# Optimization experiments

Measured on AMD Instinct MI355X. Metric: run time of the kernel, lower is better.

The kernel has to match this reference:

```python
import jax, jax.numpy as jnp
import numpy as np

N = 100000
E = 3200000
G = 64  # number of graphs


def _lin_params(key, fan_in, fan_out):
    k1, k2 = jax.random.split(key)
    bound = 1.0 / np.sqrt(fan_in)
    W = jax.random.uniform(k1, (fan_in, fan_out), jnp.float32, -bound, bound)
    b = jax.random.uniform(k2, (fan_out,), jnp.float32, -bound, bound)
    return W, b


def setup_inputs() -> dict:
    key = jax.random.key(0)
    ks = jax.random.split(key, 12)
    x = jax.random.normal(ks[0], (N, 3), jnp.float32)
    edge_index = jax.random.randint(ks[1], (2, E), 0, N, jnp.int32)
    batch = jnp.sort(jax.random.randint(ks[2], (N,), 0, G, jnp.int32))
    # conv1: in=3, heads=4, out_channels=16, concat=True -> 64
    Wq1, bq1 = _lin_params(ks[3], 3, 64)
    Wk1, bk1 = _lin_params(ks[4], 3, 64)
    Wv1, bv1 = _lin_params(ks[5], 3, 64)
    Ws1, bs1 = _lin_params(ks[6], 3, 64)
    # conv2: in=64, heads=1, out_channels=6, concat=False -> 6
    Wq2, bq2 = _lin_params(ks[7], 64, 6)
    Wk2, bk2 = _lin_params(ks[8], 64, 6)
    Wv2, bv2 = _lin_params(ks[9], 64, 6)
    Ws2, bs2 = _lin_params(ks[10], 64, 6)
    return dict(x=x, edge_index=edge_index, batch=batch,
                Wq1=Wq1, bq1=bq1, Wk1=Wk1, bk1=bk1, Wv1=Wv1, bv1=bv1, Ws1=Ws1, bs1=bs1,
                Wq2=Wq2, bq2=bq2, Wk2=Wk2, bk2=bk2, Wv2=Wv2, bv2=bv2, Ws2=Ws2, bs2=bs2)


def transformer_conv(x, src, dst, Wq, bq, Wk, bk, Wv, bv, Ws, bs, heads, d, concat):
    n = x.shape[0]
    q = (x @ Wq + bq).reshape(n, heads, d)
    k = (x @ Wk + bk).reshape(n, heads, d)
    v = (x @ Wv + bv).reshape(n, heads, d)
    # per-edge attention logits: query at target, key at source  [E, H]
    logits = jnp.einsum('ehd,ehd->eh', q[dst], k[src]) / jnp.sqrt(jnp.float32(d))
    # segment softmax over incoming edges of each target node
    m = jax.ops.segment_max(logits, dst, num_segments=n)          # [N, H]
    a = jnp.exp(logits - m[dst])                                   # [E, H]
    denom = jax.ops.segment_sum(a, dst, num_segments=n)           # [N, H]
    alpha = a / (denom[dst] + 1e-16)
    out = jax.ops.segment_sum(alpha[:, :, None] * v[src], dst, num_segments=n)  # [N,H,d]
    out = out.reshape(n, heads * d) if concat else out.mean(axis=1)
    return out + x @ Ws + bs  # root/skip connection


def reference(x, edge_index, batch,
              Wq1, bq1, Wk1, bk1, Wv1, bv1, Ws1, bs1,
              Wq2, bq2, Wk2, bk2, Wv2, bv2, Ws2, bs2):
    src, dst = edge_index[0], edge_index[1]
    h = transformer_conv(x, src, dst, Wq1, bq1, Wk1, bk1, Wv1, bv1, Ws1, bs1,
                         heads=4, d=16, concat=True)
    h = jax.nn.relu(h)
    # dropout is identity in eval mode
    h = transformer_conv(h, src, dst, Wq2, bq2, Wk2, bk2, Wv2, bv2, Ws2, bs2,
                         heads=1, d=6, concat=False)
    # global mean pool over graphs
    sums = jax.ops.segment_sum(h, batch, num_segments=G)
    cnts = jax.ops.segment_sum(jnp.ones((h.shape[0],), h.dtype), batch, num_segments=G)
    pooled = sums / jnp.maximum(cnts, 1.0)[:, None]
    return jax.nn.log_softmax(pooled, axis=1)
```

## Files before the change

### kernel.cpp

```cpp
#include <hip/hip_runtime.h>
#include <hip/hip_fp16.h>
#include <math.h>

#define N_NODES 100000
#define N_EDGES 3200000
#define N_GRAPHS 64
#define NEG_INF -1e30f

#define NB 196
#define CAP 18432
#define NBLK 1024
#define CHUNK 3125

__device__ __forceinline__ void atomAddF(float* p, float v) {
#if defined(__HIP_PLATFORM_AMD__)
    unsafeAtomicAdd(p, v);
#else
    atomicAdd(p, v);
#endif
}

__device__ __forceinline__ float b2f(unsigned w, int sh) {
    return (float)(signed char)(w >> sh);
}

__device__ __forceinline__ float kvdot(const float* q, uint4 w, float* sv_out) {
    float2 s = __half22float2(*(const __half2*)&w.w);
    *sv_out = s.y;
    return s.x * (q[0] * b2f(w.x, 0) + q[1] * b2f(w.x, 8)
                + q[2] * b2f(w.x, 16) + q[3] * b2f(w.x, 24)
                + q[4] * b2f(w.y, 0) + q[5] * b2f(w.y, 8));
}

__global__ void k0_packx(const float* __restrict__ x, float4* __restrict__ xp,
                         uint2* __restrict__ xh) {
    int n = blockIdx.x * 256 + threadIdx.x;
    if (n >= N_NODES) return;
    float x0 = x[3 * n], x1 = x[3 * n + 1], x2 = x[3 * n + 2];
    xp[n] = make_float4(x0, x1, x2, 0.f);
    __half2 h01 = __floats2half2_rn(x0, x1);
    __half2 h2p = __floats2half2_rn(x2, 0.f);
    xh[n] = make_uint2(*(unsigned*)&h01, *(unsigned*)&h2p);
}

__global__ void s1_partition(const int* __restrict__ ei,
                             int* __restrict__ bucket_fill,
                             unsigned* __restrict__ pairs) {
    __shared__ int cnt[NB];
    __shared__ int cur[NB];
    for (int i = threadIdx.x; i < NB; i += 256) cnt[i] = 0;
    __syncthreads();
    int base = blockIdx.x * CHUNK;
    for (int i = threadIdx.x; i < CHUNK; i += 256) {
        unsigned dst = (unsigned)ei[N_EDGES + base + i];
        atomicAdd(&cnt[dst >> 9], 1);
    }
    __syncthreads();
    for (int b = threadIdx.x; b < NB; b += 256) {
        int c = cnt[b];
        int off = c > 0 ? atomicAdd(&bucket_fill[b], c) : 0;
        cur[b] = b * CAP + off;
    }
    __syncthreads();
    for (int i = threadIdx.x; i < CHUNK; i += 256) {
        unsigned dst = (unsigned)ei[N_EDGES + base + i];
        int src = ei[base + i];
        int pos = atomicAdd(&cur[dst >> 9], 1);
        pairs[pos] = ((unsigned)src << 9) | (dst & 511u);
    }
}

__global__ void b4_build(const unsigned* __restrict__ pairs,
                         const int* __restrict__ bucket_fill,
                         int* __restrict__ rs, int* __restrict__ re,
                         int* __restrict__ csr_src) {
    __shared__ int cnt[512];
    __shared__ int sc[512];
    __shared__ int cur[512];
    int b = blockIdx.x;
    int tid = threadIdx.x;
    int rbase = b * CAP;
    int ne = bucket_fill[b];

    cnt[tid] = 0;
    __syncthreads();
    for (int i = tid; i < ne; i += 512)
        atomicAdd(&cnt[pairs[rbase + i] & 511u], 1);
    __syncthreads();
    sc[tid] = cnt[tid];
    __syncthreads();
    for (int off = 1; off < 512; off <<= 1) {
        int v = (tid >= off) ? sc[tid - off] : 0;
        __syncthreads();
        sc[tid] += v;
        __syncthreads();
    }
    int excl = sc[tid] - cnt[tid];
    cur[tid] = rbase + excl;
    int node = (b << 9) + tid;
    if (node < N_NODES) {
        rs[node] = rbase + excl;
        re[node] = rbase + sc[tid];
    }
    __syncthreads();
    for (int i = tid; i < ne; i += 512) {
        unsigned p = pairs[rbase + i];
        int pos = atomicAdd(&cur[p & 511u], 1);
        csr_src[pos] = (int)(p >> 9);
    }
}

__global__ void g1_layer1(const float4* __restrict__ xp,
                          const uint2* __restrict__ xh,
                          const float* __restrict__ Wq, const float* __restrict__ bq,
                          const float* __restrict__ Wk, const float* __restrict__ bk,
                          const float* __restrict__ Wv, const float* __restrict__ bv,
                          const float* __restrict__ Ws, const float* __restrict__ bs,
                          const int* __restrict__ rs, const int* __restrict__ re,
                          const int* __restrict__ csr_src,
                          uint2* __restrict__ h1) {
    __shared__ float sWq[192], sWk[192], sWv[192], sWs[192];
    __shared__ float sbq[64], sbk[64], sbv[64], sbs[64];
    for (int i = threadIdx.x; i < 192; i += 256) {
        sWq[i] = Wq[i]; sWk[i] = Wk[i]; sWv[i] = Wv[i]; sWs[i] = Ws[i];
    }
    for (int i = threadIdx.x; i < 64; i += 256) {
        sbq[i] = bq[i]; sbk[i] = bk[i]; sbv[i] = bv[i]; sbs[i] = bs[i];
    }
    __syncthreads();

    int lane = threadIdx.x & 63;
    int u = lane & 15;
    int slot = u >> 2;
    int j0 = u * 4;
    int n = blockIdx.x * 16 + (threadIdx.x >> 6) * 4 + (lane >> 4);

    float4 xc = xp[n];
    float x0 = xc.x, x1 = xc.y, x2 = xc.z;

    float q[4];
#pragma unroll
    for (int i = 0; i < 4; ++i)
        q[i] = 0.25f * (sbq[j0 + i] + x0 * sWq[j0 + i] + x1 * sWq[64 + j0 + i]
                        + x2 * sWq[128 + j0 + i]);
    float t0 = 0.f, t1 = 0.f, t2 = 0.f, tb = 0.f;
#pragma unroll
    for (int i = 0; i < 4; ++i) {
        float qi = q[i];
        t0 += qi * sWk[j0 + i];
        t1 += qi * sWk[64 + j0 + i];
        t2 += qi * sWk[128 + j0 + i];
        tb += qi * sbk[j0 + i];
    }
#pragma unroll
    for (int off = 1; off <= 2; off <<= 1) {
        t0 += __shfl_xor(t0, off);
        t1 += __shfl_xor(t1, off);
        t2 += __shfl_xor(t2, off);
        tb += __shfl_xor(tb, off);
    }
    int tsrc = (lane & 48) | ((lane & 3) << 2) | ((lane >> 2) & 3);
    t0 = __shfl(t0, tsrc, 64);
    t1 = __shfl(t1, tsrc, 64);
    t2 = __shfl(t2, tsrc, 64);
    tb = __shfl(tb, tsrc, 64);

    int row = rs[n];
    int deg = re[n] - row;

    float mA = NEG_INF, dA = 0.f, s0A = 0.f, s1A = 0.f, s2A = 0.f;
    float mB = NEG_INF, dB = 0.f, s0B = 0.f, s1B = 0.f, s2B = 0.f;
    for (int base = 0; base < deg; base += 8) {
        int eA = base + slot, eB = base + 4 + slot;
        bool vA = eA < deg, vB = eB < deg;
        int srcA = vA ? csr_src[row + eA] : 0;
        int srcB = vB ? csr_src[row + eB] : 0;
        uint2 wA = xh[srcA];
        uint2 wB = xh[srcB];
        float2 a01 = __half22float2(*(const __half2*)&wA.x);
        float a2 = __half22float2(*(const __half2*)&wA.y).x;
        float2 b01 = __half22float2(*(const __half2*)&wB.x);
        float b2 = __half22float2(*(const __half2*)&wB.y).x;
        float lA = vA ? (tb + a01.x * t0 + a01.y * t1 + a2 * t2) : NEG_INF;
        float lB = vB ? (tb + b01.x * t0 + b01.y * t1 + b2 * t2) : NEG_INF;
        float mnA = fmaxf(mA, lA);
        float scA = __expf(mA - mnA);
        float aA = vA ? __expf(lA - mnA) : 0.f;
        dA = dA * scA + aA;
        s0A = s0A * scA + aA * a01.x;
        s1A = s1A * scA + aA * a01.y;
        s2A = s2A * scA + aA * a2;
        mA = mnA;
        float mnB = fmaxf(mB, lB);
        float scB = __expf(mB - mnB);
        float aB = vB ? __expf(lB - mnB) : 0.f;
        dB = dB * scB + aB;
        s0B = s0B * scB + aB * b01.x;
        s1B = s1B * scB + aB * b01.y;
        s2B = s2B * scB + aB * b2;
        mB = mnB;
    }
    float m = fmaxf(mA, mB);
    float fA = __expf(mA - m), fB = __expf(mB - m);
    float d = dA * fA + dB * fB;
    float s0 = s0A * fA + s0B * fB;
    float s1 = s1A * fA + s1B * fB;
    float s2 = s2A * fA + s2B * fB;

    float gm = m;
    gm = fmaxf(gm, __shfl_xor(gm, 4));
    gm = fmaxf(gm, __shfl_xor(gm, 8));
    float f = __expf(m - gm);
    d *= f; s0 *= f; s1 *= f; s2 *= f;
#pragma unroll
    for (int off = 4; off <= 8; off <<= 1) {
        d += __shfl_xor(d, off);
        s0 += __shfl_xor(s0, off);
        s1 += __shfl_xor(s1, off);
        s2 += __shfl_xor(s2, off);
    }

    int esrc = (lane & 48) | ((lane >> 2) & 3);
    float dH = __shfl(d, esrc, 64);
    float s0H = __shfl(s0, esrc, 64);
    float s1H = __shfl(s1, esrc, 64);
    float s2H = __shfl(s2, esrc, 64);
    float inv = 1.f / (dH + 1e-16f);
    float fr = dH * inv, r0 = s0H * inv, r1 = s1H * inv, r2 = s2H * inv;

    float o[4];
#pragma unroll
    for (int i = 0; i < 4; ++i) {
        int j = j0 + i;
        float val = fr * sbv[j] + r0 * sWv[j] + r1 * sWv[64 + j] + r2 * sWv[128 + j]
                  + sbs[j] + x0 * sWs[j] + x1 * sWs[64 + j] + x2 * sWs[128 + j];
        o[i] = fmaxf(val, 0.f);
    }
    __half2 p01 = __floats2half2_rn(o[0], o[1]);
    __half2 p23 = __floats2half2_rn(o[2], o[3]);
    h1[(size_t)n * 16 + u] = make_uint2(*(unsigned*)&p01, *(unsigned*)&p23);
}

__global__ void k5_node2(const unsigned* __restrict__ h1,
                         const float* __restrict__ Wq, const float* __restrict__ bq,
                         const float* __restrict__ Wk, const float* __restrict__ bk,
                         const float* __restrict__ Wv, const float* __restrict__ bv,
                         const float* __restrict__ Ws, const float* __restrict__ bs,
                         float* __restrict__ q2, float* __restrict__ s2,
                         uint4* __restrict__ kv2) {
    __shared__ float sWq[384], sWk[384], sWv[384], sWs[384];
    __shared__ float sbq[6], sbk[6], sbv[6], sbs[6];
    for (int i = threadIdx.x; i < 384; i += blockDim.x) {
        sWq[i] = Wq[i]; sWk[i] = Wk[i]; sWv[i] = Wv[i]; sWs[i] = Ws[i];
    }
    if (threadIdx.x < 6) {
        sbq[threadIdx.x] = bq[threadIdx.x];
        sbk[threadIdx.x] = bk[threadIdx.x];
        sbv[threadIdx.x] = bv[threadIdx.x];
        sbs[threadIdx.x] = bs[threadIdx.x];
    }
    __syncthreads();
    int n = blockIdx.x * blockDim.x + threadIdx.x;
    if (n >= N_NODES) return;
    float qa[6], ka[6], va[6], sa[6];
#pragma unroll
    for (int c = 0; c < 6; ++c) { qa[c] = sbq[c]; ka[c] = sbk[c]; va[c] = sbv[c]; sa[c] = sbs[c]; }
    const uint4* hp = reinterpret_cast<const uint4*>(h1 + (size_t)n * 32);
#pragma unroll
    for (int i4 = 0; i4 < 8; ++i4) {
        uint4 hv = hp[i4];
        float2 f01 = __half22float2(*(const __half2*)&hv.x);
        float2 f23 = __half22float2(*(const __half2*)&hv.y);
        float2 f45 = __half22float2(*(const __half2*)&hv.z);
        float2 f67 = __half22float2(*(const __half2*)&hv.w);
        float hvv[8] = {f01.x, f01.y, f23.x, f23.y, f45.x, f45.y, f67.x, f67.y};
#pragma unroll
        for (int uu = 0; uu < 8; ++uu) {
            float hx = hvv[uu];
            int i = i4 * 8 + uu;
#pragma unroll
            for (int c = 0; c < 6; ++c) {
                qa[c] += hx * sWq[i * 6 + c];
                ka[c] += hx * sWk[i * 6 + c];
                va[c] += hx * sWv[i * 6 + c];
                sa[c] += hx * sWs[i * 6 + c];
            }
        }
    }
    const float rsqrt6 = 0.4082482904638631f;
#pragma unroll
    for (int c = 0; c < 6; ++c) {
        q2[(size_t)n * 6 + c] = qa[c] * rsqrt6;
        s2[(size_t)n * 6 + c] = sa[c];
    }
    float mk = 0.f, mv = 0.f;
#pragma unroll
    for (int c = 0; c < 6; ++c) {
        mk = fmaxf(mk, fabsf(ka[c]));
        mv = fmaxf(mv, fabsf(va[c]));
    }
    float sk = fmaxf(mk, 1e-8f) * (1.f / 127.f);
    float sv = fmaxf(mv, 1e-8f) * (1.f / 127.f);
    float isk = 1.f / sk, isv = 1.f / sv;
    int qk[6], qv[6];
#pragma unroll
    for (int c = 0; c < 6; ++c) {
        qk[c] = __float2int_rn(ka[c] * isk);
        qv[c] = __float2int_rn(va[c] * isv);
    }
    uint4 w;
    w.x = (qk[0] & 255) | ((qk[1] & 255) << 8) | ((qk[2] & 255) << 16) | ((qk[3] & 255) << 24);
    w.y = (qk[4] & 255) | ((qk[5] & 255) << 8) | ((qv[0] & 255) << 16) | ((qv[1] & 255) << 24);
    w.z = (qv[2] & 255) | ((qv[3] & 255) << 8) | ((qv[4] & 255) << 16) | ((qv[5] & 255) << 24);
    __half2 hs = __floats2half2_rn(sk, sv);
    w.w = *(unsigned*)&hs;
    kv2[n] = w;
}

__global__ void g2_layer2(const int* __restrict__ rs, const int* __restrict__ re,
                          const int* __restrict__ csr_src,
                          const float* __restrict__ q2,
                          const uint4* __restrict__ kv2,
                          const float* __restrict__ s2,
                          const int* __restrict__ batch,
                          float* __restrict__ psum, float* __restrict__ pcnt) {
    __shared__ float bsum[N_GRAPHS * 6];
    __shared__ float bcnt[N_GRAPHS];
    for (int i = threadIdx.x; i < N_GRAPHS * 6; i += 256) bsum[i] = 0.f;
    for (int i = threadIdx.x; i < N_GRAPHS; i += 256) bcnt[i] = 0.f;
    __syncthreads();

    int node = blockIdx.x * 32 + (threadIdx.x >> 3);
    int lane8 = threadIdx.x & 7;

    float q[6];
#pragma unroll
    for (int c = 0; c < 6; ++c) q[c] = q2[(size_t)node * 6 + c];
    int row = rs[node];
    int deg = re[node] - row;

    float lg[8], svr[8];
    unsigned py[8], pz[8];
#pragma unroll
    for (int i = 0; i < 8; ++i) { lg[i] = NEG_INF; svr[i] = 0.f; py[i] = 0u; pz[i] = 0u; }
    float lmax = NEG_INF;
#pragma unroll
    for (int i = 0; i < 4; ++i) {
        int e = lane8 + i * 8;
        bool v = e < deg;
        int src = v ? csr_src[row + e] : 0;
        uint4 w = kv2[src];
        float svx;
        float l = kvdot(q, w, &svx);
        if (v) {
            lg[i] = l; svr[i] = svx; py[i] = w.y; pz[i] = w.z;
            lmax = fmaxf(lmax, l);
        }
    }
    if (deg > 32) {
#pragma unroll
        for (int i = 4; i < 8; ++i) {
            int e = lane8 + i * 8;
            bool v = e < deg;
            int src = v ? csr_src[row + e] : 0;
            uint4 w = kv2[src];
            float svx;
            float l = kvdot(q, w, &svx);
            if (v) {
                lg[i] = l; svr[i] = svx; py[i] = w.y; pz[i] = w.z;
                lmax = fmaxf(lmax, l);
            }
        }
    }
    float mo = NEG_INF, dov = 0.f;
    float ao[6] = {0.f, 0.f, 0.f, 0.f, 0.f, 0.f};
    for (int e = lane8 + 64; e < deg; e += 8) {
        int src = csr_src[row + e];
        uint4 w = kv2[src];
        float svx;
        float l = kvdot(q, w, &svx);
        float mn = fmaxf(mo, l);
        float scp = __expf(mo - mn);
        float wx = __expf(l - mn);
        float wsx = wx * svx;
        dov = dov * scp + wx;
        ao[0] = ao[0] * scp + wsx * b2f(w.y, 16);
        ao[1] = ao[1] * scp + wsx * b2f(w.y, 24);
        ao[2] = ao[2] * scp + wsx * b2f(w.z, 0);
        ao[3] = ao[3] * scp + wsx * b2f(w.z, 8);
        ao[4] = ao[4] * scp + wsx * b2f(w.z, 16);
        ao[5] = ao[5] * scp + wsx * b2f(w.z, 24);
        mo = mn;
    }
    lmax = fmaxf(lmax, mo);
    lmax = fmaxf(lmax, __shfl_xor(lmax, 1));
    lmax = fmaxf(lmax, __shfl_xor(lmax, 2));
    lmax = fmaxf(lmax, __shfl_xor(lmax, 4));
    if (lmax < -5e29f) lmax = 0.f;

    float d = 0.f;
    float acc[6] = {0.f, 0.f, 0.f, 0.f, 0.f, 0.f};
#pragma unroll
    for (int i = 0; i < 8; ++i) {
        float w = __expf(lg[i] - lmax);
        float ws = w * svr[i];
        d += w;
        acc[0] += ws * b2f(py[i], 16);
        acc[1] += ws * b2f(py[i], 24);
        acc[2] += ws * b2f(pz[i], 0);
        acc[3] += ws * b2f(pz[i], 8);
        acc[4] += ws * b2f(pz[i], 16);
        acc[5] += ws * b2f(pz[i], 24);
    }
    float so = __expf(mo - lmax);
    d += dov * so;
#pragma unroll
    for (int c = 0; c < 6; ++c) acc[c] += ao[c] * so;

#pragma unroll
    for (int off = 1; off <= 4; off <<= 1) {
        d += __shfl_xor(d, off);
#pragma unroll
        for (int c = 0; c < 6; ++c) acc[c] += __shfl_xor(acc[c], off);
    }

    if (lane8 == 0) {
        float inv = 1.f / (d + 1e-16f);
        int g = batch[node];
#pragma unroll
        for (int c = 0; c < 6; ++c) {
            float val = acc[c] * inv + s2[(size_t)node * 6 + c];
            atomicAdd(&bsum[g * 6 + c], val);
        }
        atomicAdd(&bcnt[g], 1.f);
    }
    __syncthreads();
    for (int i = threadIdx.x; i < N_GRAPHS * 6; i += 256) {
        float v = bsum[i];
        if (v != 0.f) atomAddF(psum + i, v);
    }
    for (int i = threadIdx.x; i < N_GRAPHS; i += 256) {
        float v = bcnt[i];
        if (v != 0.f) atomAddF(pcnt + i, v);
    }
}

__global__ void k9_final(const float* __restrict__ psum, const float* __restrict__ pcnt,
                         float* __restrict__ out) {
    int g = threadIdx.x;
    if (g >= N_GRAPHS) return;
    float cnt = fmaxf(pcnt[g], 1.0f);
    float z[6];
    float mx = -1e30f;
#pragma unroll
    for (int c = 0; c < 6; ++c) {
        z[c] = psum[g * 6 + c] / cnt;
        mx = fmaxf(mx, z[c]);
    }
    float se = 0.f;
#pragma unroll
    for (int c = 0; c < 6; ++c) se += __expf(z[c] - mx);
    float lse = mx + logf(se);
#pragma unroll
    for (int c = 0; c < 6; ++c) out[g * 6 + c] = z[c] - lse;
}

extern "C" void kernel_launch(void* const* d_in, const int* in_sizes, int n_in,
                              void* d_out, int out_size, void* d_ws, size_t ws_size,
                              hipStream_t stream) {
    const float* x   = (const float*)d_in[0];
    const int*   ei  = (const int*)d_in[1];
    const int*   bat = (const int*)d_in[2];
    const float* Wq1 = (const float*)d_in[3];  const float* bq1 = (const float*)d_in[4];
    const float* Wk1 = (const float*)d_in[5];  const float* bk1 = (const float*)d_in[6];
    const float* Wv1 = (const float*)d_in[7];  const float* bv1 = (const float*)d_in[8];
    const float* Ws1 = (const float*)d_in[9];  const float* bs1 = (const float*)d_in[10];
    const float* Wq2 = (const float*)d_in[11]; const float* bq2 = (const float*)d_in[12];
    const float* Wk2 = (const float*)d_in[13]; const float* bk2 = (const float*)d_in[14];
    const float* Wv2 = (const float*)d_in[15]; const float* bv2 = (const float*)d_in[16];
    const float* Ws2 = (const float*)d_in[17]; const float* bs2 = (const float*)d_in[18];
    float* out = (float*)d_out;

    char* ws = (char*)d_ws;
    size_t off = 0;
    auto alloc = [&](size_t bytes) -> char* {
        char* p = ws + off;
        off += (bytes + 255) & ~(size_t)255;
        return p;
    };

    float* psum = (float*)alloc((size_t)N_GRAPHS * 6 * 4);
    float* pcnt = (float*)alloc((size_t)N_GRAPHS * 4);
    int* bucket_fill = (int*)alloc((size_t)NB * 4);
    size_t zero_bytes = off;

    unsigned* pairs   = (unsigned*)alloc((size_t)NB * CAP * 4);
    int*      csr_src = (int*)     alloc((size_t)NB * CAP * 4);
    int*      rsv     = (int*)     alloc((size_t)N_NODES * 4);
    int*      rev     = (int*)     alloc((size_t)N_NODES * 4);
    float4*   xp      = (float4*)  alloc((size_t)N_NODES * 16);
    uint2*    xh      = (uint2*)   alloc((size_t)N_NODES * 8);
    unsigned* h1      = (unsigned*)alloc((size_t)N_NODES * 64 * 2);
    float*    q2      = (float*)   alloc((size_t)N_NODES * 6 * 4);
    float*    s2      = (float*)   alloc((size_t)N_NODES * 6 * 4);
    uint4*    kv2     = (uint4*)   alloc((size_t)N_NODES * 16);

    hipMemsetAsync(d_ws, 0, zero_bytes, stream);

    k0_packx<<<(N_NODES + 255) / 256, 256, 0, stream>>>(x, xp, xh);
    s1_partition<<<NBLK, 256, 0, stream>>>(ei, bucket_fill, pairs);
    b4_build<<<NB, 512, 0, stream>>>(pairs, bucket_fill, rsv, rev, csr_src);

    g1_layer1<<<N_NODES / 16, 256, 0, stream>>>(xp, xh, Wq1, bq1, Wk1, bk1, Wv1, bv1,
                                                Ws1, bs1, rsv, rev, csr_src,
                                                (uint2*)h1);
    k5_node2<<<(N_NODES + 255) / 256, 256, 0, stream>>>(h1, Wq2, bq2, Wk2, bk2,
                                                        Wv2, bv2, Ws2, bs2,
                                                        q2, s2, kv2);
    g2_layer2<<<N_NODES / 32, 256, 0, stream>>>(rsv, rev, csr_src, q2, kv2, s2,
                                                bat, psum, pcnt);
    k9_final<<<1, 64, 0, stream>>>(psum, pcnt, out);
}
```

Baseline: 168.5 us.

## Sort edge chunks locally in LDS and replace global bucket atomics with per-block offsets

The partition kernel now sorts each block's chunk of edges by destination bucket in shared memory, writes the sorted chunk contiguously, and records per-block bucket offsets. This replaces global atomics on bucket fill counters and scattered writes. The build kernel then gathers each bucket's segments from all 512 blocks using those offsets, one wave per segment. This yields coalesced writes in partitioning, at the cost of fragmented short-segment reads in the build step and heavy shared memory use per block.

```diff
diff --git a/kernel.cpp b/kernel.cpp
--- a/kernel.cpp
+++ b/kernel.cpp
@@ -9,8 +9,8 @@
 
 #define NB 196
 #define CAP 18432
-#define NBLK 1024
-#define CHUNK 3125
+#define NBLK 512
+#define CHUNK 6250
 
 __device__ __forceinline__ void atomAddF(float* p, float v) {
 #if defined(__HIP_PLATFORM_AMD__)
@@ -43,49 +43,75 @@
     xh[n] = make_uint2(*(unsigned*)&h01, *(unsigned*)&h2p);
 }
 
-__global__ void s1_partition(const int* __restrict__ ei,
-                             int* __restrict__ bucket_fill,
-                             unsigned* __restrict__ pairs) {
-    __shared__ int cnt[NB];
-    __shared__ int cur[NB];
-    for (int i = threadIdx.x; i < NB; i += 256) cnt[i] = 0;
-    __syncthreads();
-    int base = blockIdx.x * CHUNK;
-    for (int i = threadIdx.x; i < CHUNK; i += 256) {
-        unsigned dst = (unsigned)ei[N_EDGES + base + i];
-        atomicAdd(&cnt[dst >> 9], 1);
-    }
-    __syncthreads();
-    for (int b = threadIdx.x; b < NB; b += 256) {
-        int c = cnt[b];
-        int off = c > 0 ? atomicAdd(&bucket_fill[b], c) : 0;
-        cur[b] = b * CAP + off;
-    }
-    __syncthreads();
-    for (int i = threadIdx.x; i < CHUNK; i += 256) {
-        unsigned dst = (unsigned)ei[N_EDGES + base + i];
-        int src = ei[base + i];
-        int pos = atomicAdd(&cur[dst >> 9], 1);
-        pairs[pos] = ((unsigned)src << 9) | (dst & 511u);
-    }
-}
-
-__global__ void b4_build(const unsigned* __restrict__ pairs,
-                         const int* __restrict__ bucket_fill,
-                         int* __restrict__ rs, int* __restrict__ re,
-                         int* __restrict__ csr_src) {
-    __shared__ int cnt[512];
-    __shared__ int sc[512];
-    __shared__ int cur[512];
+__global__ __launch_bounds__(512) void s1_partition(const int* __restrict__ ei,
+                                                    int* __restrict__ offs,
+                                                    unsigned* __restrict__ pairs) {
+    __shared__ unsigned pairbuf[CHUNK];
+    __shared__ unsigned sortbuf[CHUNK];
+    __shared__ unsigned char buckbuf[CHUNK];
+    __shared__ int hist[4][200];
+    __shared__ int cur[NB], tmp[NB];
+    int tid = threadIdx.x;
+    int wp = tid >> 7;
+    for (int i = tid; i < 4 * 200; i += 512) ((int*)hist)[i] = 0;
+    __syncthreads();
+    int gbase = blockIdx.x * CHUNK;
+    for (int i = tid; i < CHUNK; i += 512) {
+        int src = ei[gbase + i];
+        unsigned dst = (unsigned)ei[N_EDGES + gbase + i];
+        pairbuf[i] = ((unsigned)src << 9) | (dst & 511u);
+        unsigned b = dst >> 9;
+        buckbuf[i] = (unsigned char)b;
+        atomicAdd(&hist[wp][b], 1);
+    }
+    __syncthreads();
+    if (tid < NB)
+        tmp[tid] = hist[0][tid] + hist[1][tid] + hist[2][tid] + hist[3][tid];
+    __syncthreads();
+    for (int off = 1; off < NB; off <<= 1) {
+        int v = 0;
+        if (tid < NB && tid >= off) v = tmp[tid - off];
+        __syncthreads();
+        if (tid < NB) tmp[tid] += v;
+        __syncthreads();
+    }
+    if (tid < NB) {
+        int cnt_b = hist[0][tid] + hist[1][tid] + hist[2][tid] + hist[3][tid];
+        int excl = tmp[tid] - cnt_b;
+        cur[tid] = excl;
+        offs[blockIdx.x * NB + tid] = excl;
+    }
+    __syncthreads();
+    for (int i = tid; i < CHUNK; i += 512) {
+        int pos = atomicAdd(&cur[buckbuf[i]], 1);
+        sortbuf[pos] = pairbuf[i];
+    }
+    __syncthreads();
+    for (int i = tid; i < CHUNK; i += 512)
+        pairs[gbase + i] = sortbuf[i];
+}
+
+__global__ __launch_bounds__(512) void b4_build(const unsigned* __restrict__ pairs,
+                                                const int* __restrict__ offs,
+                                                int* __restrict__ rs,
+                                                int* __restrict__ re,
+                                                int* __restrict__ csr_src) {
+    __shared__ int so[NBLK], seg_e[NBLK];
+    __shared__ int cnt[512], sc[512], cur[512];
     int b = blockIdx.x;
     int tid = threadIdx.x;
-    int rbase = b * CAP;
-    int ne = bucket_fill[b];
-
+    for (int k = tid; k < NBLK; k += 512) {
+        so[k] = offs[k * NB + b];
+        seg_e[k] = (b == NB - 1) ? CHUNK : offs[k * NB + b + 1];
+    }
     cnt[tid] = 0;
     __syncthreads();
-    for (int i = tid; i < ne; i += 512)
-        atomicAdd(&cnt[pairs[rbase + i] & 511u], 1);
+    int wave = tid >> 6, lane = tid & 63;
+    for (int k = wave; k < NBLK; k += 8) {
+        int s = so[k], e = seg_e[k], gb = k * CHUNK;
+        for (int i = s + lane; i < e; i += 64)
+            atomicAdd(&cnt[pairs[gb + i] & 511u], 1);
+    }
     __syncthreads();
     sc[tid] = cnt[tid];
     __syncthreads();
@@ -95,6 +121,7 @@
         sc[tid] += v;
         __syncthreads();
     }
+    int rbase = b * CAP;
     int excl = sc[tid] - cnt[tid];
     cur[tid] = rbase + excl;
     int node = (b << 9) + tid;
@@ -103,10 +130,13 @@
         re[node] = rbase + sc[tid];
     }
     __syncthreads();
-    for (int i = tid; i < ne; i += 512) {
-        unsigned p = pairs[rbase + i];
-        int pos = atomicAdd(&cur[p & 511u], 1);
-        csr_src[pos] = (int)(p >> 9);
+    for (int k = wave; k < NBLK; k += 8) {
+        int s = so[k], e = seg_e[k], gb = k * CHUNK;
+        for (int i = s + lane; i < e; i += 64) {
+            unsigned p = pairs[gb + i];
+            int pos = atomicAdd(&cur[p & 511u], 1);
+            csr_src[pos] = (int)(p >> 9);
+        }
     }
 }
 
@@ -491,10 +521,10 @@
 
     float* psum = (float*)alloc((size_t)N_GRAPHS * 6 * 4);
     float* pcnt = (float*)alloc((size_t)N_GRAPHS * 4);
-    int* bucket_fill = (int*)alloc((size_t)NB * 4);
     size_t zero_bytes = off;
 
-    unsigned* pairs   = (unsigned*)alloc((size_t)NB * CAP * 4);
+    int*      offs    = (int*)     alloc((size_t)NBLK * NB * 4);
+    unsigned* pairs   = (unsigned*)alloc((size_t)N_EDGES * 4);
     int*      csr_src = (int*)     alloc((size_t)NB * CAP * 4);
     int*      rsv     = (int*)     alloc((size_t)N_NODES * 4);
     int*      rev     = (int*)     alloc((size_t)N_NODES * 4);
@@ -508,8 +538,8 @@
     hipMemsetAsync(d_ws, 0, zero_bytes, stream);
 
     k0_packx<<<(N_NODES + 255) / 256, 256, 0, stream>>>(x, xp, xh);
-    s1_partition<<<NBLK, 256, 0, stream>>>(ei, bucket_fill, pairs);
-    b4_build<<<NB, 512, 0, stream>>>(pairs, bucket_fill, rsv, rev, csr_src);
+    s1_partition<<<NBLK, 512, 0, stream>>>(ei, offs, pairs);
+    b4_build<<<NB, 512, 0, stream>>>(pairs, offs, rsv, rev, csr_src);
 
     g1_layer1<<<N_NODES / 16, 256, 0, stream>>>(xp, xh, Wq1, bq1, Wk1, bk1, Wv1, bv1,
                                                 Ws1, bs1, rsv, rev, csr_src,
```

Result: faster. 163.4 us (-3.0%).
